# Performance work log

Measured on AMD Instinct MI355X. Metric: run time of the kernel, lower is better.

The kernel has to match this reference:

```python
import jax, jax.numpy as jnp
import numpy as np

FG_IOU = 0.7
BG_IOU = 0.3
IMG_H = 640.0
IMG_W = 640.0


def setup_inputs() -> dict:
    key = jax.random.key(0)
    k1, k2, k3, k4 = jax.random.split(key, 4)
    B, A, G = 8, 184320, 64
    # anchors in cxcywh (as the torch module assumes before box_convert)
    cxcy = jax.random.uniform(k1, (B, A, 2), dtype=jnp.float32) * 640.0
    wh = 16.0 + jax.random.uniform(k2, (B, A, 2), dtype=jnp.float32) * 240.0
    anchors = jnp.concatenate([cxcy, wh], axis=-1)
    # gt boxes in xyxy, inside the 640x640 image
    xy1 = jax.random.uniform(k3, (B, G, 2), dtype=jnp.float32) * 560.0
    wh_g = 24.0 + jax.random.uniform(k4, (B, G, 2), dtype=jnp.float32) * 180.0
    gt_boxes = jnp.concatenate([xy1, jnp.minimum(xy1 + wh_g, 640.0)], axis=-1)
    return {"anchors": anchors, "gt_boxes": gt_boxes}


def cxcywh_to_xyxy(b):
    cx, cy, w, h = b[..., 0], b[..., 1], b[..., 2], b[..., 3]
    return jnp.stack([cx - 0.5 * w, cy - 0.5 * h, cx + 0.5 * w, cy + 0.5 * h], axis=-1)


def box_iou(a, g):
    # a: [A,4] xyxy, g: [G,4] xyxy -> [A,G]
    area_a = (a[:, 2] - a[:, 0]) * (a[:, 3] - a[:, 1])
    area_g = (g[:, 2] - g[:, 0]) * (g[:, 3] - g[:, 1])
    lt = jnp.maximum(a[:, None, :2], g[None, :, :2])   # [A,G,2]
    rb = jnp.minimum(a[:, None, 2:], g[None, :, 2:])
    wh = jnp.clip(rb - lt, 0.0)
    inter = wh[..., 0] * wh[..., 1]
    return inter / (area_a[:, None] + area_g[None, :] - inter)


def _assign_one(anchors_cxcywh, gt):
    # anchors_cxcywh: [A,4], gt: [G,4] xyxy
    A = anchors_cxcywh.shape[0]
    a = cxcywh_to_xyxy(anchors_cxcywh)                 # [A,4]
    iou = box_iou(a, gt)                               # [A,G]

    labels = jnp.full((A,), -1, dtype=jnp.int32)
    matched = jnp.zeros((A, 4), dtype=anchors_cxcywh.dtype)

    # rule 1: for each gt, the anchor attaining its max IoU is positive
    best_anchor = jnp.argmax(iou, axis=0)              # [G]
    labels = labels.at[best_anchor].set(1)
    matched = matched.at[best_anchor].set(gt)

    # rule 2: anchors with max IoU over gts > fg threshold are positive
    max_gt = jnp.argmax(iou, axis=1)                   # [A]
    max_val = jnp.max(iou, axis=1)                     # [A]
    fg = max_val > FG_IOU
    labels = jnp.where(fg, 1, labels)
    matched = jnp.where(fg[:, None], gt[max_gt], matched)

    # rule 3: remaining anchors with max IoU < bg threshold are negative
    bg = (max_val < BG_IOU) & (labels < 0)
    labels = jnp.where(bg, 0, labels)

    # filter cross-boundary anchors -> ignore label
    cross = (a[:, 0] < 0) | (a[:, 1] < 0) | (a[:, 2] > IMG_W) | (a[:, 3] > IMG_H)
    labels = jnp.where(cross, -1, labels)
    return labels, matched, max_val


def reference(anchors, gt_boxes):
    # anchors: [B,A,4] cxcywh, gt_boxes: [B,G,4] xyxy
    labels, matched_bboxes, max_iou = jax.vmap(_assign_one)(anchors, gt_boxes)
    return labels, matched_bboxes, max_iou
```

## Files before the change

kernel.cpp:

```cpp
#include <hip/hip_runtime.h>


constexpr int B = 8;
constexpr int G = 64;
constexpr int BLOCK = 256;
constexpr int APT = 3;
constexpr int ABLK = BLOCK * APT;
constexpr int NSTRIP = 128;
constexpr float STRIP_SCALE = 0.2f;
constexpr float STRIP_W = 5.0f;
constexpr float IMG = 640.0f;
constexpr float FG_IOU = 0.7f;
constexpr float BG_IOU = 0.3f;
constexpr float SLACK = 1.0f;
constexpr unsigned long long KEY_INIT = 0xFFFFFFFFull;


__global__ __launch_bounds__(512) void build_tables(
    const float4* __restrict__ gt, unsigned long long* __restrict__ tabs) {
    __shared__ float4 sgt[G];
    const int b = blockIdx.x;
    const int t = threadIdx.x;
    if (t < G) sgt[t] = gt[b * G + t];
    __syncthreads();
    const int tabIdx = t >> 7;
    const int strip = t & 127;
    const int comp = (tabIdx == 0) ? 0 : (tabIdx == 1) ? 2 : (tabIdx == 2) ? 1 : 3;
    const bool hi = (tabIdx & 1) != 0;
    const float thr = hi ? (strip * STRIP_W - SLACK)
                         : ((strip + 1) * STRIP_W + SLACK);
    unsigned long long m = 0ull;
    for (int g = 0; g < G; ++g) {
        float c = ((const float*)&sgt[g])[comp];
        bool in = hi ? (c > thr) : (c < thr);
        if (in) m |= (1ull << g);
    }
    tabs[(size_t)b * 512 + t] = m;
}

__global__ __launch_bounds__(BLOCK) void assign_main(
    const float4* __restrict__ anchors,
    const float4* __restrict__ gt,
    float* __restrict__ L,
    float4* __restrict__ M,
    float* __restrict__ V,
    long long* __restrict__ gkeys,
    const unsigned long long* __restrict__ tabs,
    int A, int bpb) {
#pragma clang fp contract(off)
    __shared__ float sgx0[G], sgy0[G], sgx1[G], sgy1[G], sga[G];
    __shared__ unsigned long long tab[4][NSTRIP];
    __shared__ unsigned long long skey[G];

    const int b = blockIdx.x / bpb;
    const int t = threadIdx.x;
    const int base = (blockIdx.x % bpb) * ABLK;

    if (t < G) {
        float4 gb = gt[b * G + t];
        sgx0[t] = gb.x; sgy0[t] = gb.y; sgx1[t] = gb.z; sgy1[t] = gb.w;
        sga[t] = (gb.z - gb.x) * (gb.w - gb.y);
        skey[t] = KEY_INIT;
    }
    {
        const ulonglong2* src = (const ulonglong2*)(tabs + (size_t)b * 512);
        ((ulonglong2*)&tab[0][0])[t] = src[t];
    }
    __syncthreads();

    float4 anbuf[APT];
    size_t idxs[APT];
    int as[APT];
#pragma unroll
    for (int j = 0; j < APT; ++j) {
        as[j] = base + j * BLOCK + t;
        idxs[j] = (size_t)b * A + as[j];
        anbuf[j] = anchors[idxs[j]];
    }

#pragma unroll
    for (int j = 0; j < APT; ++j) {
        const int a = as[j];
        const size_t idx = idxs[j];
        const float4 an = anbuf[j];
        float ax0 = an.x - 0.5f * an.z;
        float ay0 = an.y - 0.5f * an.w;
        float ax1 = an.x + 0.5f * an.z;
        float ay1 = an.y + 0.5f * an.w;
        float area_a = (ax1 - ax0) * (ay1 - ay0);

        int sx0 = (int)(ax0 * STRIP_SCALE); sx0 = sx0 < 0 ? 0 : (sx0 > 127 ? 127 : sx0);
        int sx1 = (int)(ax1 * STRIP_SCALE); sx1 = sx1 < 0 ? 0 : (sx1 > 127 ? 127 : sx1);
        int sy0 = (int)(ay0 * STRIP_SCALE); sy0 = sy0 < 0 ? 0 : (sy0 > 127 ? 127 : sy0);
        int sy1 = (int)(ay1 * STRIP_SCALE); sy1 = sy1 < 0 ? 0 : (sy1 > 127 ? 127 : sy1);

        unsigned long long mask =
            tab[0][sx1] & tab[1][sx0] & tab[2][sy1] & tab[3][sy0];

        float maxv = 0.0f;
        int maxg = 0;
        const unsigned long long inv_p =
            (unsigned long long)(0xFFFFFFFFu - (unsigned)a);

        auto half = [&](unsigned m, int gbase) {
            while (m) {
                const int g1 = gbase + (int)__builtin_ctz(m);
                m &= m - 1;
                const int cand = gbase + (int)__builtin_ctz(m | 0x80000000u);
                const int g2 = m ? cand : g1;
                m &= m - 1;

                const float gx0a = sgx0[g1], gy0a = sgy0[g1];
                const float gx1a = sgx1[g1], gy1a = sgy1[g1];
                const float saa  = sga[g1];
                const float gx0b = sgx0[g2], gy0b = sgy0[g2];
                const float gx1b = sgx1[g2], gy1b = sgy1[g2];
                const float sab  = sga[g2];

                float lxa = fmaxf(ax0, gx0a), lya = fmaxf(ay0, gy0a);
                float rxa = fminf(ax1, gx1a), rya = fminf(ay1, gy1a);
                float wa = fmaxf(rxa - lxa, 0.0f), ha = fmaxf(rya - lya, 0.0f);
                float intera = wa * ha;
                float unia = area_a + saa - intera;
                float ioua = intera / unia;

                float lxb = fmaxf(ax0, gx0b), lyb = fmaxf(ay0, gy0b);
                float rxb = fminf(ax1, gx1b), ryb = fminf(ay1, gy1b);
                float wb = fmaxf(rxb - lxb, 0.0f), hb = fmaxf(ryb - lyb, 0.0f);
                float interb = wb * hb;
                float unib = area_a + sab - interb;
                float ioub = interb / unib;

                bool b1 = ioua > maxv;
                maxv = b1 ? ioua : maxv;
                maxg = b1 ? g1 : maxg;
                bool b2 = ioub > maxv;
                maxv = b2 ? ioub : maxv;
                maxg = b2 ? g2 : maxg;

                unsigned long long key1 =
                    ((unsigned long long)__float_as_uint(ioua) << 32) | inv_p;
                unsigned long long key2 =
                    ((unsigned long long)__float_as_uint(ioub) << 32) | inv_p;
                atomicMax(&skey[g1], key1);
                atomicMax(&skey[g2], key2);
            }
        };
        half((unsigned)mask, 0);
        half((unsigned)(mask >> 32), 32);

        bool fg = maxv > FG_IOU;
        bool bg = maxv < BG_IOU;
        bool cross = (ax0 < 0.0f) || (ay0 < 0.0f) || (ax1 > IMG) || (ay1 > IMG);

        L[idx] = cross ? -1.0f : (fg ? 1.0f : (bg ? 0.0f : -1.0f));
        float4 mbox = make_float4(0.0f, 0.0f, 0.0f, 0.0f);
        if (fg)
            mbox = make_float4(sgx0[maxg], sgy0[maxg], sgx1[maxg], sgy1[maxg]);
        M[idx] = mbox;
        V[idx] = maxv;
    }

    __syncthreads();
    if (t < G) {
        atomicMax(&gkeys[b * G + t], (long long)skey[t]);
    }
}

__global__ void fixup(
    const float4* __restrict__ anchors,
    const float4* __restrict__ gt,
    const long long* __restrict__ gkeys,
    float* __restrict__ L,
    float4* __restrict__ M,
    const float* __restrict__ V,
    int A) {
#pragma clang fp contract(off)
    const int b = blockIdx.x;
    const int g = threadIdx.x;
    __shared__ int tgt[G];

    unsigned long long key = (unsigned long long)gkeys[b * G + g];
    unsigned int a = 0xFFFFFFFFu - (unsigned int)(key & 0xFFFFFFFFull);
    tgt[g] = (int)a;
    __syncthreads();

    bool write = true;
    for (int g2 = g + 1; g2 < G; ++g2)
        if (tgt[g2] == (int)a) { write = false; break; }
    if (!write) return;

    const size_t idx = (size_t)b * A + a;
    float4 an = anchors[idx];
    float ax0 = an.x - 0.5f * an.z;
    float ay0 = an.y - 0.5f * an.w;
    float ax1 = an.x + 0.5f * an.z;
    float ay1 = an.y + 0.5f * an.w;
    bool cross = (ax0 < 0.0f) || (ay0 < 0.0f) || (ax1 > IMG) || (ay1 > IMG);
    L[idx] = cross ? -1.0f : 1.0f;
    if (!(V[idx] > FG_IOU)) M[idx] = gt[b * G + g];
}

extern "C" void kernel_launch(void* const* d_in, const int* in_sizes, int n_in,
                              void* d_out, int out_size, void* d_ws, size_t ws_size,
                              hipStream_t stream) {
    const float4* anchors = (const float4*)d_in[0];
    const float4* gt      = (const float4*)d_in[1];
    const int A = in_sizes[0] / (B * 4);

    float* out = (float*)d_out;
    float*  L = out;
    float4* M = (float4*)(out + (size_t)B * A);
    float*  V = out + (size_t)B * A * 5;

    char* ws = (char*)d_ws;
    long long* gkeys = (long long*)(ws + 256);
    unsigned long long* tabs = (unsigned long long*)(ws + 8192);

    const int bpb = A / ABLK;
    build_tables<<<B, 512, 0, stream>>>(gt, tabs);
    assign_main<<<B * bpb, BLOCK, 0, stream>>>(anchors, gt, L, M, V, gkeys,
                                               tabs, A, bpb);
    fixup<<<B, G, 0, stream>>>(anchors, gt, gkeys, L, M, V, A);
}
```

Before: 121.0 us.

## Sort anchors by candidate count within block to reduce wavefront divergence

Each block now computes every anchor's candidate GT mask first and stores the boxes and masks in shared memory. It then counting-sorts the block's anchors by mask popcount, using a histogram and a wavefront prefix scan, and reassigns them to threads. Anchors with similar loop trip counts thus land in the same wavefront, which cuts idle lanes in the divergent IoU loop. The cost is extra shared memory, several barriers, shared atomics, and scattered, uncoalesced global output writes.

```diff
diff --git a/kernel.cpp b/kernel.cpp
--- a/kernel.cpp
+++ b/kernel.cpp
@@ -14,6 +14,7 @@
 constexpr float BG_IOU = 0.3f;
 constexpr float SLACK = 1.0f;
 constexpr unsigned long long KEY_INIT = 0xFFFFFFFFull;
+constexpr unsigned long long TOPBIT = 0x8000000000000000ull;
 
 
 __global__ __launch_bounds__(512) void build_tables(
@@ -51,6 +52,11 @@
     __shared__ float sgx0[G], sgy0[G], sgx1[G], sgy1[G], sga[G];
     __shared__ unsigned long long tab[4][NSTRIP];
     __shared__ unsigned long long skey[G];
+    __shared__ float sax0[ABLK], say0[ABLK], sax1[ABLK], say1[ABLK];
+    __shared__ unsigned long long smask[ABLK];
+    __shared__ unsigned short sidx[ABLK];
+    __shared__ int hist[G];
+    __shared__ int pfx[G];
 
     const int b = blockIdx.x / bpb;
     const int t = threadIdx.x;
@@ -61,97 +67,119 @@
         sgx0[t] = gb.x; sgy0[t] = gb.y; sgx1[t] = gb.z; sgy1[t] = gb.w;
         sga[t] = (gb.z - gb.x) * (gb.w - gb.y);
         skey[t] = KEY_INIT;
+        hist[t] = 0;
     }
     {
         const ulonglong2* src = (const ulonglong2*)(tabs + (size_t)b * 512);
         ((ulonglong2*)&tab[0][0])[t] = src[t];
     }
-    __syncthreads();
 
     float4 anbuf[APT];
-    size_t idxs[APT];
-    int as[APT];
+#pragma unroll
+    for (int j = 0; j < APT; ++j)
+        anbuf[j] = anchors[(size_t)b * A + base + j * BLOCK + t];
+
+    __syncthreads();
+
+    int pops[APT];
 #pragma unroll
     for (int j = 0; j < APT; ++j) {
-        as[j] = base + j * BLOCK + t;
-        idxs[j] = (size_t)b * A + as[j];
-        anbuf[j] = anchors[idxs[j]];
-    }
-
-#pragma unroll
-    for (int j = 0; j < APT; ++j) {
-        const int a = as[j];
-        const size_t idx = idxs[j];
+        const int k = j * BLOCK + t;
         const float4 an = anbuf[j];
-        float ax0 = an.x - 0.5f * an.z;
-        float ay0 = an.y - 0.5f * an.w;
-        float ax1 = an.x + 0.5f * an.z;
-        float ay1 = an.y + 0.5f * an.w;
-        float area_a = (ax1 - ax0) * (ay1 - ay0);
+        const float ax0 = an.x - 0.5f * an.z;
+        const float ay0 = an.y - 0.5f * an.w;
+        const float ax1 = an.x + 0.5f * an.z;
+        const float ay1 = an.y + 0.5f * an.w;
+        sax0[k] = ax0; say0[k] = ay0; sax1[k] = ax1; say1[k] = ay1;
 
         int sx0 = (int)(ax0 * STRIP_SCALE); sx0 = sx0 < 0 ? 0 : (sx0 > 127 ? 127 : sx0);
         int sx1 = (int)(ax1 * STRIP_SCALE); sx1 = sx1 < 0 ? 0 : (sx1 > 127 ? 127 : sx1);
         int sy0 = (int)(ay0 * STRIP_SCALE); sy0 = sy0 < 0 ? 0 : (sy0 > 127 ? 127 : sy0);
         int sy1 = (int)(ay1 * STRIP_SCALE); sy1 = sy1 < 0 ? 0 : (sy1 > 127 ? 127 : sy1);
-
-        unsigned long long mask =
+        const unsigned long long mask =
             tab[0][sx1] & tab[1][sx0] & tab[2][sy1] & tab[3][sy0];
+        smask[k] = mask;
+        pops[j] = __builtin_popcountll(mask);
+        atomicAdd(&hist[pops[j] > 63 ? 63 : pops[j]], 1);
+    }
+    __syncthreads();
+
+    if (t < G) {
+        const int c0 = hist[t];
+        int x = c0;
+#pragma unroll
+        for (int d = 1; d < 64; d <<= 1) {
+            int y = __shfl_up(x, d, 64);
+            if (t >= d) x += y;
+        }
+        pfx[t] = x - c0;
+    }
+    __syncthreads();
+
+#pragma unroll
+    for (int j = 0; j < APT; ++j) {
+        const int bin = pops[j] > 63 ? 63 : pops[j];
+        const int pos = atomicAdd(&pfx[bin], 1);
+        sidx[pos] = (unsigned short)(j * BLOCK + t);
+    }
+    __syncthreads();
+
+#pragma unroll
+    for (int r = 0; r < APT; ++r) {
+        const int k = (int)sidx[r * BLOCK + t];
+        const int a = base + k;
+        const size_t idx = (size_t)b * A + a;
+        const float ax0 = sax0[k], ay0 = say0[k];
+        const float ax1 = sax1[k], ay1 = say1[k];
+        const float area_a = (ax1 - ax0) * (ay1 - ay0);
+        unsigned long long m = smask[k];
 
         float maxv = 0.0f;
         int maxg = 0;
         const unsigned long long inv_p =
             (unsigned long long)(0xFFFFFFFFu - (unsigned)a);
 
-        auto half = [&](unsigned m, int gbase) {
-            while (m) {
-                const int g1 = gbase + (int)__builtin_ctz(m);
-                m &= m - 1;
-                const int cand = gbase + (int)__builtin_ctz(m | 0x80000000u);
-                const int g2 = m ? cand : g1;
-                m &= m - 1;
-
-                const float gx0a = sgx0[g1], gy0a = sgy0[g1];
-                const float gx1a = sgx1[g1], gy1a = sgy1[g1];
-                const float saa  = sga[g1];
-                const float gx0b = sgx0[g2], gy0b = sgy0[g2];
-                const float gx1b = sgx1[g2], gy1b = sgy1[g2];
-                const float sab  = sga[g2];
-
-                float lxa = fmaxf(ax0, gx0a), lya = fmaxf(ay0, gy0a);
-                float rxa = fminf(ax1, gx1a), rya = fminf(ay1, gy1a);
-                float wa = fmaxf(rxa - lxa, 0.0f), ha = fmaxf(rya - lya, 0.0f);
-                float intera = wa * ha;
-                float unia = area_a + saa - intera;
-                float ioua = intera / unia;
-
-                float lxb = fmaxf(ax0, gx0b), lyb = fmaxf(ay0, gy0b);
-                float rxb = fminf(ax1, gx1b), ryb = fminf(ay1, gy1b);
-                float wb = fmaxf(rxb - lxb, 0.0f), hb = fmaxf(ryb - lyb, 0.0f);
-                float interb = wb * hb;
-                float unib = area_a + sab - interb;
-                float ioub = interb / unib;
-
-                bool b1 = ioua > maxv;
-                maxv = b1 ? ioua : maxv;
-                maxg = b1 ? g1 : maxg;
-                bool b2 = ioub > maxv;
-                maxv = b2 ? ioub : maxv;
-                maxg = b2 ? g2 : maxg;
-
-                unsigned long long key1 =
-                    ((unsigned long long)__float_as_uint(ioua) << 32) | inv_p;
-                unsigned long long key2 =
-                    ((unsigned long long)__float_as_uint(ioub) << 32) | inv_p;
-                atomicMax(&skey[g1], key1);
-                atomicMax(&skey[g2], key2);
-            }
-        };
-        half((unsigned)mask, 0);
-        half((unsigned)(mask >> 32), 32);
-
-        bool fg = maxv > FG_IOU;
-        bool bg = maxv < BG_IOU;
-        bool cross = (ax0 < 0.0f) || (ay0 < 0.0f) || (ax1 > IMG) || (ay1 > IMG);
+        while (m) {
+            const int g1 = (int)__builtin_ctzll(m);          m &= m - 1;
+            const int cand = (int)__builtin_ctzll(m | TOPBIT);
+            const int g2 = m ? cand : g1;                    m &= m - 1;
+
+            const float gx0a = sgx0[g1], gy0a = sgy0[g1];
+            const float gx1a = sgx1[g1], gy1a = sgy1[g1];
+            const float saa  = sga[g1];
+            const float gx0b = sgx0[g2], gy0b = sgy0[g2];
+            const float gx1b = sgx1[g2], gy1b = sgy1[g2];
+            const float sab  = sga[g2];
+
+            float lxa = fmaxf(ax0, gx0a), lya = fmaxf(ay0, gy0a);
+            float rxa = fminf(ax1, gx1a), rya = fminf(ay1, gy1a);
+            float wa = fmaxf(rxa - lxa, 0.0f), ha = fmaxf(rya - lya, 0.0f);
+            float intera = wa * ha;
+            float unia = area_a + saa - intera;
+            float ioua = intera / unia;
+
+            float lxb = fmaxf(ax0, gx0b), lyb = fmaxf(ay0, gy0b);
+            float rxb = fminf(ax1, gx1b), ryb = fminf(ay1, gy1b);
+            float wb = fmaxf(rxb - lxb, 0.0f), hb = fmaxf(ryb - lyb, 0.0f);
+            float interb = wb * hb;
+            float unib = area_a + sab - interb;
+            float ioub = interb / unib;
+
+            bool b1 = ioua > maxv; maxv = b1 ? ioua : maxv; maxg = b1 ? g1 : maxg;
+            bool b2 = ioub > maxv; maxv = b2 ? ioub : maxv; maxg = b2 ? g2 : maxg;
+
+            unsigned long long key1 =
+                ((unsigned long long)__float_as_uint(ioua) << 32) | inv_p;
+            unsigned long long key2 =
+                ((unsigned long long)__float_as_uint(ioub) << 32) | inv_p;
+            atomicMax(&skey[g1], key1);
+            atomicMax(&skey[g2], key2);
+        }
+
+        const bool fg = maxv > FG_IOU;
+        const bool bg = maxv < BG_IOU;
+        const bool cross =
+            (ax0 < 0.0f) || (ay0 < 0.0f) || (ax1 > IMG) || (ay1 > IMG);
 
         L[idx] = cross ? -1.0f : (fg ? 1.0f : (bg ? 0.0f : -1.0f));
         float4 mbox = make_float4(0.0f, 0.0f, 0.0f, 0.0f);
```

After: 116.9 us. -3.3%, faster.
